# Optimization experiments

Measured on AMD Instinct MI355X. Metric: run time of the kernel, lower is better.

The kernel has to match this reference:

```python
import jax, jax.numpy as jnp
import numpy as np

B, T, D_EMBED, HEAD = 8, 4096, 128, 64


def setup_inputs() -> dict:
    key = jax.random.key(0)
    k1, k2, k3, k4 = jax.random.split(key, 4)
    x = jax.random.normal(k1, (B, T, D_EMBED), dtype=jnp.float32)
    # torch nn.Linear(d_embed, head_size, bias=False): y = x @ W^T, W:[head,in].
    # We store W already transposed as [in, head] for x @ W.
    Wq = jax.random.normal(k2, (D_EMBED, HEAD), dtype=jnp.float32) * (1.0 / np.sqrt(D_EMBED))
    Wk = jax.random.normal(k3, (D_EMBED, HEAD), dtype=jnp.float32) * (1.0 / np.sqrt(D_EMBED))
    Wv = jax.random.normal(k4, (D_EMBED, HEAD), dtype=jnp.float32) * (1.0 / np.sqrt(D_EMBED))
    return {"x": x, "Wq": Wq, "Wk": Wk, "Wv": Wv}


def reference(x, Wq, Wk, Wv):
    # x: [B, T, D]; projections to [B, T, H]
    T_ = x.shape[1]
    D_ = x.shape[2]
    Q = x @ Wq
    K = x @ Wk
    V = x @ Wv
    # NOTE: source divides by sqrt(feature_dimension) == sqrt(d_embed), not head_size
    scores = jnp.einsum('bqh,bkh->bqk', Q, K) / jnp.sqrt(jnp.float32(D_))
    causal = jnp.tril(jnp.ones((T_, T_), dtype=bool))  # [T, T]
    scores = jnp.where(causal[None, :, :], scores, -jnp.inf)
    probs = jax.nn.softmax(scores, axis=-1)  # [B, T, T]
    return jnp.einsum('bqk,bkh->bqh', probs, V)
```

## Files before the change

### kernel.cpp

```cpp
#include <hip/hip_runtime.h>
#include <hip/hip_bf16.h>

typedef __attribute__((ext_vector_type(8))) short bf16x8;
typedef __attribute__((ext_vector_type(4))) short short4v;
typedef __attribute__((ext_vector_type(4))) float f32x4;

#define MFMA16(a, b, c) __builtin_amdgcn_mfma_f32_16x16x32_bf16((a), (b), (c), 0, 0, 0)

#if __has_builtin(__builtin_amdgcn_mfma_f32_16x16x16bf16_1k)
#define HAVE_X16 1
#define MFMAX16(a, b, c) __builtin_amdgcn_mfma_f32_16x16x16bf16_1k((a), (b), (c), 0, 0, 0)
#elif __has_builtin(__builtin_amdgcn_mfma_f32_16x16x16_bf16)
#define HAVE_X16 1
#define MFMAX16(a, b, c) __builtin_amdgcn_mfma_f32_16x16x16_bf16((a), (b), (c), 0, 0, 0)
#else
#define HAVE_X16 0
#endif

constexpr int Bn = 8, Tn = 4096, Dn = 128, Hn = 64;

__device__ inline unsigned short f2b(float f) {
    union { float f; unsigned u; } v; v.f = f;
    unsigned r = v.u + 0x7fff + ((v.u >> 16) & 1);
    return (unsigned short)(r >> 16);
}
#if __has_builtin(__builtin_amdgcn_cvt_pk_bf16_f32)
typedef __attribute__((ext_vector_type(2))) __bf16 bf16x2_t;
__device__ inline unsigned pk2(float a, float b) {
    union { bf16x2_t v; unsigned u; } c;
    c.v = __builtin_amdgcn_cvt_pk_bf16_f32(a, b);
    return c.u;
}
#else
__device__ inline unsigned pk2(float a, float b) {
    return (unsigned)f2b(a) | ((unsigned)f2b(b) << 16);
}
#endif
__device__ inline short4v pk4(float a, float b, float c, float d) {
    union { unsigned u[2]; short4v s; } r;
    r.u[0] = pk2(a, b); r.u[1] = pk2(c, d);
    return r.s;
}

__global__ __launch_bounds__(256) void qkv(const float* __restrict__ X,
                                           const float* __restrict__ Wq,
                                           const float* __restrict__ Wk,
                                           const float* __restrict__ Wv,
                                           unsigned short* __restrict__ Qp,
                                           unsigned short* __restrict__ Kp,
                                           unsigned short* __restrict__ VTp,
                                           float* __restrict__ Out,
                                           float* __restrict__ Lsum,
                                           int* __restrict__ cnt) {
    __shared__ unsigned short xt[64 * 136];
    __shared__ unsigned short wt[64 * 136];
    __shared__ unsigned short ot[64 * 72];
    int tid = threadIdx.x, w = tid >> 6, lane = tid & 63, quad = lane >> 4, l15 = lane & 15;
    int g = blockIdx.x;
    int m0 = g * 64;
    int b = m0 >> 12, tloc = m0 & (Tn - 1);
    const float kLog2Scale = 0.12751879523175464f;

    #pragma unroll
    for (int i = 0; i < 4; i++)
        *(f32x4*)&Out[(size_t)g * 4096 + (size_t)(tid + i * 256) * 4] = (f32x4){0.f, 0.f, 0.f, 0.f};
    if (tid < 64) Lsum[g * 64 + tid] = 0.f;
    if (g == 0) { cnt[tid] = 0; cnt[tid + 256] = 0; }

    #pragma unroll
    for (int c = 0; c < 8; c++) {
        int e = tid * 4 + c * 1024;
        int row = e >> 7, col = e & 127;
        f32x4 v = *(const f32x4*)&X[(size_t)(m0 + row) * Dn + col];
        *(short4v*)&xt[row * 136 + col] = pk4(v[0], v[1], v[2], v[3]);
    }
    __syncthreads();

    bf16x8 a[4];
    #pragma unroll
    for (int kt = 0; kt < 4; kt++)
        a[kt] = *(const bf16x8*)&xt[(w * 16 + l15) * 136 + kt * 32 + quad * 8];

    for (int mat = 0; mat < 3; mat++) {
        const float* W = (mat == 0) ? Wq : (mat == 1) ? Wk : Wv;
        __syncthreads();
        #pragma unroll
        for (int ps = 0; ps < 8; ps++) {
            int k = (tid >> 4) + ps * 16;
            int n4 = (tid & 15) * 4;
            f32x4 wv = *(const f32x4*)&W[k * Hn + n4];
            wt[(n4 + 0) * 136 + k] = f2b(wv[0]);
            wt[(n4 + 1) * 136 + k] = f2b(wv[1]);
            wt[(n4 + 2) * 136 + k] = f2b(wv[2]);
            wt[(n4 + 3) * 136 + k] = f2b(wv[3]);
        }
        __syncthreads();

        f32x4 acc[4];
        #pragma unroll
        for (int nt = 0; nt < 4; nt++) {
            acc[nt] = (f32x4){0.f, 0.f, 0.f, 0.f};
            const unsigned short* wtm = &wt[(nt * 16 + l15) * 136 + quad * 8];
            #pragma unroll
            for (int kt = 0; kt < 4; kt++)
                acc[nt] = MFMA16(a[kt], *(const bf16x8*)&wtm[kt * 32], acc[nt]);
        }
        __syncthreads();
        if (mat < 2) {
            float sc = (mat == 0) ? kLog2Scale : 1.0f;
            #pragma unroll
            for (int nt = 0; nt < 4; nt++)
                #pragma unroll
                for (int rg = 0; rg < 4; rg++)
                    ot[(w * 16 + quad * 4 + rg) * 72 + nt * 16 + l15] = f2b(acc[nt][rg] * sc);
        } else {
            #pragma unroll
            for (int nt = 0; nt < 4; nt++)
                *(short4v*)&ot[(nt * 16 + l15) * 72 + w * 16 + quad * 4] =
                    pk4(acc[nt][0], acc[nt][1], acc[nt][2], acc[nt][3]);
        }
        __syncthreads();
        if (mat < 2) {
            unsigned short* O = mat ? Kp : Qp;
            #pragma unroll
            for (int i = 0; i < 2; i++) {
                int row = (tid >> 3) + 32 * i, ch8 = tid & 7;
                *(bf16x8*)&O[(size_t)(m0 + row) * Hn + ch8 * 8] = *(const bf16x8*)&ot[row * 72 + ch8 * 8];
            }
        } else {
            #pragma unroll
            for (int i = 0; i < 2; i++) {
                int h = (tid >> 3) + 32 * i, ch8 = tid & 7;
                *(bf16x8*)&VTp[((size_t)(b * Hn + h)) * Tn + tloc + ch8 * 8] = *(const bf16x8*)&ot[h * 72 + ch8 * 8];
            }
        }
    }
}

__global__ __launch_bounds__(256) void attn(const unsigned short* __restrict__ Qp,
                                            const unsigned short* __restrict__ Kp,
                                            const unsigned short* __restrict__ VTp,
                                            float* __restrict__ Out,
                                            float* __restrict__ Lsum,
                                            int* __restrict__ cnt) {
    __shared__ __align__(16) char shmem[18432];
    unsigned short* Ks = (unsigned short*)shmem;
    unsigned short* Vs = Ks + 64 * 72;
#if !HAVE_X16
    __shared__ __align__(16) unsigned short Ps[4][32 * 40];
#endif
    __shared__ float Lbuf[2][64];
    __shared__ int lastflag;

    int idx = blockIdx.x;
    int b = idx & 7;
    int c = 159 - (idx >> 3);
    int qt, ch, nch;
    if (c < 16)      { qt = c;                 ch = 0;          nch = 1; }
    else if (c < 48) { int t = c - 16; qt = 16 + (t >> 1); ch = t & 1;      nch = 2; }
    else if (c < 96) { int t = c - 48; int q3 = t / 3; qt = 32 + q3; ch = t - 3 * q3; nch = 3; }
    else             { int t = c - 96; qt = 48 + (t >> 2); ch = t & 3;      nch = 4; }
    int k0 = ch * 16, k1 = min(qt, k0 + 15);

    int tid = threadIdx.x, w = tid >> 6, lane = tid & 63, quad = lane >> 4, l15 = lane & 15;
    int qh = w & 1, kh = w >> 1;
    int Q0 = qt * 64;
    const unsigned short* Kb = Kp + (size_t)b * Tn * Hn;
    const unsigned short* Vb = VTp + (size_t)b * Hn * Tn;

    int srow = tid >> 3, scol = (tid & 7) * 8;
    const f32x4* Ksrc = (const f32x4*)Kb;

    f32x4 kr[2], vr[2];
    #pragma unroll
    for (int i = 0; i < 2; i++) kr[i] = Ksrc[k0 * 512 + tid + i * 256];
    #pragma unroll
    for (int i = 0; i < 2; i++) vr[i] = *(const f32x4*)&Vb[(size_t)(srow + i * 32) * Tn + k0 * 64 + scol];

    bf16x8 qf[2][2];
    {
        const unsigned short* Qb = Qp + ((size_t)b * Tn + Q0 + qh * 32) * Hn;
        #pragma unroll
        for (int nq = 0; nq < 2; nq++)
            #pragma unroll
            for (int hc = 0; hc < 2; hc++)
                qf[nq][hc] = *(const bf16x8*)&Qb[(nq * 16 + l15) * Hn + hc * 32 + quad * 8];
    }

    f32x4 o[2][4];
    #pragma unroll
    for (int nq = 0; nq < 2; nq++)
        #pragma unroll
        for (int nh = 0; nh < 4; nh++) o[nq][nh] = (f32x4){0.f, 0.f, 0.f, 0.f};
    float li[2] = {0.f, 0.f};

    for (int kt = k0; kt <= k1; kt++) {
        __syncthreads();
        #pragma unroll
        for (int i = 0; i < 2; i++) *(f32x4*)&Ks[(srow + i * 32) * 72 + scol] = kr[i];
        #pragma unroll
        for (int i = 0; i < 2; i++) *(f32x4*)&Vs[(srow + i * 32) * 72 + scol] = vr[i];
        __syncthreads();
        if (kt < k1) {
            #pragma unroll
            for (int i = 0; i < 2; i++) kr[i] = Ksrc[(kt + 1) * 512 + tid + i * 256];
            #pragma unroll
            for (int i = 0; i < 2; i++)
                vr[i] = *(const f32x4*)&Vb[(size_t)(srow + i * 32) * Tn + (kt + 1) * 64 + scol];
        }

        bf16x8 kf[2][2];
        #pragma unroll
        for (int mt = 0; mt < 2; mt++)
            #pragma unroll
            for (int hc = 0; hc < 2; hc++)
                kf[mt][hc] = *(const bf16x8*)&Ks[(kh * 32 + mt * 16 + l15) * 72 + hc * 32 + quad * 8];

        f32x4 s[2][2];
        #pragma unroll
        for (int mt = 0; mt < 2; mt++)
            #pragma unroll
            for (int nq = 0; nq < 2; nq++) {
                f32x4 acc = {0.f, 0.f, 0.f, 0.f};
                acc = MFMA16(kf[mt][0], qf[nq][0], acc);
                acc = MFMA16(kf[mt][1], qf[nq][1], acc);
                s[mt][nq] = acc;
            }

        bool diag = (kt == qt);
        int kbase = kt * 64 + kh * 32 + quad * 4;
        int qbase = Q0 + qh * 32 + l15;

#if HAVE_X16
        short4v vB[2][4];
        #pragma unroll
        for (int mt = 0; mt < 2; mt++)
            #pragma unroll
            for (int nh = 0; nh < 4; nh++)
                vB[mt][nh] = *(const short4v*)&Vs[(nh * 16 + l15) * 72 + kh * 32 + mt * 16 + quad * 4];
        short4v pkv[2][2];
        #pragma unroll
        for (int mt = 0; mt < 2; mt++) {
            #pragma unroll
            for (int nq = 0; nq < 2; nq++) {
                float p[4];
                #pragma unroll
                for (int rg = 0; rg < 4; rg++) {
                    float pe = __builtin_amdgcn_exp2f(s[mt][nq][rg]);
                    if (diag && (kbase + mt * 16 + rg > qbase + nq * 16)) pe = 0.f;
                    li[nq] += pe;
                    p[rg] = pe;
                }
                pkv[mt][nq] = pk4(p[0], p[1], p[2], p[3]);
            }
        }
        #pragma unroll
        for (int mt = 0; mt < 2; mt++)
            #pragma unroll
            for (int nq = 0; nq < 2; nq++)
                #pragma unroll
                for (int nh = 0; nh < 4; nh++)
                    o[nq][nh] = MFMAX16(pkv[mt][nq], vB[mt][nh], o[nq][nh]);
#else
        bf16x8 vf[4];
        #pragma unroll
        for (int nh = 0; nh < 4; nh++)
            vf[nh] = *(const bf16x8*)&Vs[(nh * 16 + l15) * 72 + kh * 32 + quad * 8];
        unsigned short* Pw = &Ps[w][0];
        #pragma unroll
        for (int mt = 0; mt < 2; mt++) {
            #pragma unroll
            for (int nq = 0; nq < 2; nq++) {
                float p[4];
                #pragma unroll
                for (int rg = 0; rg < 4; rg++) {
                    float pe = __builtin_amdgcn_exp2f(s[mt][nq][rg]);
                    if (diag && (kbase + mt * 16 + rg > qbase + nq * 16)) pe = 0.f;
                    li[nq] += pe;
                    p[rg] = pe;
                }
                *(short4v*)&Pw[(nq * 16 + l15) * 40 + mt * 16 + quad * 4] = pk4(p[0], p[1], p[2], p[3]);
            }
        }
        bf16x8 pf[2];
        #pragma unroll
        for (int nq = 0; nq < 2; nq++)
            pf[nq] = *(const bf16x8*)&Pw[(nq * 16 + l15) * 40 + quad * 8];
        #pragma unroll
        for (int nq = 0; nq < 2; nq++)
            #pragma unroll
            for (int nh = 0; nh < 4; nh++)
                o[nq][nh] = MFMA16(pf[nq], vf[nh], o[nq][nh]);
#endif
    }

    __syncthreads();
    float (*Cbuf)[32][66] = (float (*)[32][66])shmem;
    #pragma unroll
    for (int nq = 0; nq < 2; nq++) {
        li[nq] += __shfl_xor(li[nq], 16);
        li[nq] += __shfl_xor(li[nq], 32);
    }
    if (lane < 16) {
        Lbuf[kh][qh * 32 + lane]      = li[0];
        Lbuf[kh][qh * 32 + 16 + lane] = li[1];
    }
    if (kh == 1) {
        #pragma unroll
        for (int nq = 0; nq < 2; nq++)
            #pragma unroll
            for (int nh = 0; nh < 4; nh++)
                #pragma unroll
                for (int rg = 0; rg < 4; rg++)
                    Cbuf[qh][nq * 16 + quad * 4 + rg][nh * 16 + l15] = o[nq][nh][rg];
    }
    __syncthreads();

    if (nch == 1) {
        if (kh == 0) {
            #pragma unroll
            for (int nq = 0; nq < 2; nq++) {
                #pragma unroll
                for (int rg = 0; rg < 4; rg++) {
                    int qloc = nq * 16 + quad * 4 + rg;
                    float inv = 1.0f / (Lbuf[0][qh * 32 + qloc] + Lbuf[1][qh * 32 + qloc]);
                    size_t row = (size_t)b * Tn + Q0 + qh * 32 + qloc;
                    #pragma unroll
                    for (int nh = 0; nh < 4; nh++)
                        Out[row * Hn + nh * 16 + l15] =
                            (o[nq][nh][rg] + Cbuf[qh][qloc][nh * 16 + l15]) * inv;
                }
            }
        }
    } else {
        if (kh == 0) {
            #pragma unroll
            for (int nq = 0; nq < 2; nq++) {
                #pragma unroll
                for (int rg = 0; rg < 4; rg++) {
                    int qloc = nq * 16 + quad * 4 + rg;
                    size_t row = (size_t)b * Tn + Q0 + qh * 32 + qloc;
                    #pragma unroll
                    for (int nh = 0; nh < 4; nh++)
                        atomicAdd(&Out[row * Hn + nh * 16 + l15],
                                  o[nq][nh][rg] + Cbuf[qh][qloc][nh * 16 + l15]);
                }
            }
        }
        if (tid < 64)
            atomicAdd(&Lsum[(b << 12) + Q0 + tid], Lbuf[0][tid] + Lbuf[1][tid]);
        __threadfence_block();
        __syncthreads();
        if (tid == 0)
            lastflag = (atomicAdd(&cnt[b * 64 + qt], 1) == nch - 1);
        __syncthreads();
        if (lastflag) {
            __threadfence_block();
            size_t gbase = ((size_t)b * Tn + Q0) * Hn;
            #pragma unroll
            for (int i = 0; i < 4; i++) {
                int idx4 = tid + i * 256;
                int q = idx4 >> 4;
                float inv = 1.0f / Lsum[(b << 12) + Q0 + q];
                f32x4 v = *(f32x4*)&Out[gbase + (size_t)idx4 * 4];
                v[0] *= inv; v[1] *= inv; v[2] *= inv; v[3] *= inv;
                *(f32x4*)&Out[gbase + (size_t)idx4 * 4] = v;
            }
        }
    }
}

extern "C" void kernel_launch(void* const* d_in, const int* in_sizes, int n_in,
                              void* d_out, int out_size, void* d_ws, size_t ws_size,
                              hipStream_t stream) {
    const float* X  = (const float*)d_in[0];
    const float* Wq = (const float*)d_in[1];
    const float* Wk = (const float*)d_in[2];
    const float* Wv = (const float*)d_in[3];
    float* out = (float*)d_out;

    char* ws = (char*)d_ws;
    size_t szQ = (size_t)Bn * Tn * Hn * sizeof(unsigned short);
    unsigned short* Qp  = (unsigned short*)(ws);
    unsigned short* Kp  = (unsigned short*)(ws + szQ);
    unsigned short* VTp = (unsigned short*)(ws + 2 * szQ);
    float*          Ls  = (float*)(ws + 3 * szQ);
    int*            Ct  = (int*)(ws + 3 * szQ + (128 << 10));

    qkv<<<Bn * Tn / 64, 256, 0, stream>>>(X, Wq, Wk, Wv, Qp, Kp, VTp, out, Ls, Ct);
    attn<<<1280, 256, 0, stream>>>(Qp, Kp, VTp, out, Ls, Ct);
}
```

Before: 129.0 us.

## Double-buffer K/V tiles in LDS and spread epilogue across all warps

Converts the attention loop to double-buffered LDS so the next K/V tile is written to the alternate buffer after compute, dropping one barrier per iteration. The epilogue now has all four warps write partial outputs to LDS and each thread reduce and store or atomically add 16 contiguous values, instead of only half the warps doing the work. The projection kernel's weight transpose also packs four bf16 values per LDS store. The changes cost extra LDS and remove the non-x16 fallback path, which now silently returns the accumulator unchanged.

```diff
diff --git a/kernel.cpp b/kernel.cpp
--- a/kernel.cpp
+++ b/kernel.cpp
@@ -7,15 +7,13 @@
 
 #define MFMA16(a, b, c) __builtin_amdgcn_mfma_f32_16x16x32_bf16((a), (b), (c), 0, 0, 0)
 
+__device__ inline f32x4 mfmax16(short4v a, short4v b, f32x4 c) {
 #if __has_builtin(__builtin_amdgcn_mfma_f32_16x16x16bf16_1k)
-#define HAVE_X16 1
-#define MFMAX16(a, b, c) __builtin_amdgcn_mfma_f32_16x16x16bf16_1k((a), (b), (c), 0, 0, 0)
-#elif __has_builtin(__builtin_amdgcn_mfma_f32_16x16x16_bf16)
-#define HAVE_X16 1
-#define MFMAX16(a, b, c) __builtin_amdgcn_mfma_f32_16x16x16_bf16((a), (b), (c), 0, 0, 0)
+    return __builtin_amdgcn_mfma_f32_16x16x16bf16_1k(a, b, c, 0, 0, 0);
 #else
-#define HAVE_X16 0
+    return c;
 #endif
+}
 
 constexpr int Bn = 8, Tn = 4096, Dn = 128, Hn = 64;
 
@@ -85,14 +83,16 @@
         const float* W = (mat == 0) ? Wq : (mat == 1) ? Wk : Wv;
         __syncthreads();
         #pragma unroll
-        for (int ps = 0; ps < 8; ps++) {
-            int k = (tid >> 4) + ps * 16;
+        for (int p = 0; p < 2; p++) {
+            int kb = (tid >> 4) * 4 + p * 64;
             int n4 = (tid & 15) * 4;
-            f32x4 wv = *(const f32x4*)&W[k * Hn + n4];
-            wt[(n4 + 0) * 136 + k] = f2b(wv[0]);
-            wt[(n4 + 1) * 136 + k] = f2b(wv[1]);
-            wt[(n4 + 2) * 136 + k] = f2b(wv[2]);
-            wt[(n4 + 3) * 136 + k] = f2b(wv[3]);
+            f32x4 wv0 = *(const f32x4*)&W[(kb + 0) * Hn + n4];
+            f32x4 wv1 = *(const f32x4*)&W[(kb + 1) * Hn + n4];
+            f32x4 wv2 = *(const f32x4*)&W[(kb + 2) * Hn + n4];
+            f32x4 wv3 = *(const f32x4*)&W[(kb + 3) * Hn + n4];
+            #pragma unroll
+            for (int n = 0; n < 4; n++)
+                *(short4v*)&wt[(n4 + n) * 136 + kb] = pk4(wv0[n], wv1[n], wv2[n], wv3[n]);
         }
         __syncthreads();
 
@@ -143,12 +143,7 @@
                                             float* __restrict__ Out,
                                             float* __restrict__ Lsum,
                                             int* __restrict__ cnt) {
-    __shared__ __align__(16) char shmem[18432];
-    unsigned short* Ks = (unsigned short*)shmem;
-    unsigned short* Vs = Ks + 64 * 72;
-#if !HAVE_X16
-    __shared__ __align__(16) unsigned short Ps[4][32 * 40];
-#endif
+    __shared__ __align__(16) char shmem[2][18432];
     __shared__ float Lbuf[2][64];
     __shared__ int lastflag;
 
@@ -176,6 +171,14 @@
     for (int i = 0; i < 2; i++) kr[i] = Ksrc[k0 * 512 + tid + i * 256];
     #pragma unroll
     for (int i = 0; i < 2; i++) vr[i] = *(const f32x4*)&Vb[(size_t)(srow + i * 32) * Tn + k0 * 64 + scol];
+    {
+        unsigned short* Ks0 = (unsigned short*)&shmem[0][0];
+        unsigned short* Vs0 = Ks0 + 64 * 72;
+        #pragma unroll
+        for (int i = 0; i < 2; i++) *(f32x4*)&Ks0[(srow + i * 32) * 72 + scol] = kr[i];
+        #pragma unroll
+        for (int i = 0; i < 2; i++) *(f32x4*)&Vs0[(srow + i * 32) * 72 + scol] = vr[i];
+    }
 
     bf16x8 qf[2][2];
     {
@@ -194,20 +197,19 @@
         for (int nh = 0; nh < 4; nh++) o[nq][nh] = (f32x4){0.f, 0.f, 0.f, 0.f};
     float li[2] = {0.f, 0.f};
 
+    int cur = 0;
     for (int kt = k0; kt <= k1; kt++) {
         __syncthreads();
-        #pragma unroll
-        for (int i = 0; i < 2; i++) *(f32x4*)&Ks[(srow + i * 32) * 72 + scol] = kr[i];
-        #pragma unroll
-        for (int i = 0; i < 2; i++) *(f32x4*)&Vs[(srow + i * 32) * 72 + scol] = vr[i];
-        __syncthreads();
-        if (kt < k1) {
+        bool pref = (kt < k1);
+        if (pref) {
             #pragma unroll
             for (int i = 0; i < 2; i++) kr[i] = Ksrc[(kt + 1) * 512 + tid + i * 256];
             #pragma unroll
             for (int i = 0; i < 2; i++)
                 vr[i] = *(const f32x4*)&Vb[(size_t)(srow + i * 32) * Tn + (kt + 1) * 64 + scol];
         }
+        unsigned short* Ks = (unsigned short*)&shmem[cur][0];
+        unsigned short* Vs = Ks + 64 * 72;
 
         bf16x8 kf[2][2];
         #pragma unroll
@@ -231,7 +233,6 @@
         int kbase = kt * 64 + kh * 32 + quad * 4;
         int qbase = Q0 + qh * 32 + l15;
 
-#if HAVE_X16
         short4v vB[2][4];
         #pragma unroll
         for (int mt = 0; mt < 2; mt++)
@@ -260,42 +261,21 @@
             for (int nq = 0; nq < 2; nq++)
                 #pragma unroll
                 for (int nh = 0; nh < 4; nh++)
-                    o[nq][nh] = MFMAX16(pkv[mt][nq], vB[mt][nh], o[nq][nh]);
-#else
-        bf16x8 vf[4];
-        #pragma unroll
-        for (int nh = 0; nh < 4; nh++)
-            vf[nh] = *(const bf16x8*)&Vs[(nh * 16 + l15) * 72 + kh * 32 + quad * 8];
-        unsigned short* Pw = &Ps[w][0];
-        #pragma unroll
-        for (int mt = 0; mt < 2; mt++) {
-            #pragma unroll
-            for (int nq = 0; nq < 2; nq++) {
-                float p[4];
-                #pragma unroll
-                for (int rg = 0; rg < 4; rg++) {
-                    float pe = __builtin_amdgcn_exp2f(s[mt][nq][rg]);
-                    if (diag && (kbase + mt * 16 + rg > qbase + nq * 16)) pe = 0.f;
-                    li[nq] += pe;
-                    p[rg] = pe;
-                }
-                *(short4v*)&Pw[(nq * 16 + l15) * 40 + mt * 16 + quad * 4] = pk4(p[0], p[1], p[2], p[3]);
-            }
-        }
-        bf16x8 pf[2];
-        #pragma unroll
-        for (int nq = 0; nq < 2; nq++)
-            pf[nq] = *(const bf16x8*)&Pw[(nq * 16 + l15) * 40 + quad * 8];
-        #pragma unroll
-        for (int nq = 0; nq < 2; nq++)
-            #pragma unroll
-            for (int nh = 0; nh < 4; nh++)
-                o[nq][nh] = MFMA16(pf[nq], vf[nh], o[nq][nh]);
-#endif
+                    o[nq][nh] = mfmax16(pkv[mt][nq], vB[mt][nh], o[nq][nh]);
+
+        if (pref) {
+            unsigned short* Ksn = (unsigned short*)&shmem[cur ^ 1][0];
+            unsigned short* Vsn = Ksn + 64 * 72;
+            #pragma unroll
+            for (int i = 0; i < 2; i++) *(f32x4*)&Ksn[(srow + i * 32) * 72 + scol] = kr[i];
+            #pragma unroll
+            for (int i = 0; i < 2; i++) *(f32x4*)&Vsn[(srow + i * 32) * 72 + scol] = vr[i];
+            cur ^= 1;
+        }
     }
 
     __syncthreads();
-    float (*Cbuf)[32][66] = (float (*)[32][66])shmem;
+    float (*Cb)[32][66] = (float (*)[32][66])&shmem[0][0];
     #pragma unroll
     for (int nq = 0; nq < 2; nq++) {
         li[nq] += __shfl_xor(li[nq], 16);
@@ -305,48 +285,27 @@
         Lbuf[kh][qh * 32 + lane]      = li[0];
         Lbuf[kh][qh * 32 + 16 + lane] = li[1];
     }
-    if (kh == 1) {
-        #pragma unroll
-        for (int nq = 0; nq < 2; nq++)
-            #pragma unroll
-            for (int nh = 0; nh < 4; nh++)
-                #pragma unroll
-                for (int rg = 0; rg < 4; rg++)
-                    Cbuf[qh][nq * 16 + quad * 4 + rg][nh * 16 + l15] = o[nq][nh][rg];
-    }
+    #pragma unroll
+    for (int nq = 0; nq < 2; nq++)
+        #pragma unroll
+        for (int nh = 0; nh < 4; nh++)
+            #pragma unroll
+            for (int rg = 0; rg < 4; rg++)
+                Cb[kh * 2 + qh][nq * 16 + quad * 4 + rg][nh * 16 + l15] = o[nq][nh][rg];
     __syncthreads();
 
+    int row = tid >> 2, cg = (tid & 3) * 16;
+    int qh_r = row >> 5, ql_r = row & 31;
+    size_t gout = ((size_t)b * Tn + Q0 + row) * Hn + cg;
     if (nch == 1) {
-        if (kh == 0) {
-            #pragma unroll
-            for (int nq = 0; nq < 2; nq++) {
-                #pragma unroll
-                for (int rg = 0; rg < 4; rg++) {
-                    int qloc = nq * 16 + quad * 4 + rg;
-                    float inv = 1.0f / (Lbuf[0][qh * 32 + qloc] + Lbuf[1][qh * 32 + qloc]);
-                    size_t row = (size_t)b * Tn + Q0 + qh * 32 + qloc;
-                    #pragma unroll
-                    for (int nh = 0; nh < 4; nh++)
-                        Out[row * Hn + nh * 16 + l15] =
-                            (o[nq][nh][rg] + Cbuf[qh][qloc][nh * 16 + l15]) * inv;
-                }
-            }
-        }
+        float inv = 1.0f / (Lbuf[0][row] + Lbuf[1][row]);
+        #pragma unroll
+        for (int i = 0; i < 16; i++)
+            Out[gout + i] = (Cb[qh_r][ql_r][cg + i] + Cb[2 + qh_r][ql_r][cg + i]) * inv;
     } else {
-        if (kh == 0) {
-            #pragma unroll
-            for (int nq = 0; nq < 2; nq++) {
-                #pragma unroll
-                for (int rg = 0; rg < 4; rg++) {
-                    int qloc = nq * 16 + quad * 4 + rg;
-                    size_t row = (size_t)b * Tn + Q0 + qh * 32 + qloc;
-                    #pragma unroll
-                    for (int nh = 0; nh < 4; nh++)
-                        atomicAdd(&Out[row * Hn + nh * 16 + l15],
-                                  o[nq][nh][rg] + Cbuf[qh][qloc][nh * 16 + l15]);
-                }
-            }
-        }
+        #pragma unroll
+        for (int i = 0; i < 16; i++)
+            atomicAdd(&Out[gout + i], Cb[qh_r][ql_r][cg + i] + Cb[2 + qh_r][ql_r][cg + i]);
         if (tid < 64)
             atomicAdd(&Lsum[(b << 12) + Q0 + tid], Lbuf[0][tid] + Lbuf[1][tid]);
         __threadfence_block();
```

Result: slower. 315.8 us (+144.8%).
